# Kernel optimization log

Measured on AMD Instinct MI355X. Metric: run time of the kernel, lower is better.

## Reference

```python
import jax, jax.numpy as jnp
import numpy as np

H = 51  # hidden size fixed by the module

def _gru_cell(x, h, w_ih, w_hh, b_ih, b_hh):
    # PyTorch GRUCell math. w_ih: [3H, in], w_hh: [3H, H]
    gi = x @ w_ih.T + b_ih          # [B, 3H]
    gh = h @ w_hh.T + b_hh          # [B, 3H]
    i_r, i_z, i_n = jnp.split(gi, 3, axis=-1)
    h_r, h_z, h_n = jnp.split(gh, 3, axis=-1)
    r = jax.nn.sigmoid(i_r + h_r)
    z = jax.nn.sigmoid(i_z + h_z)
    n = jnp.tanh(i_n + r * h_n)
    return (1.0 - z) * n + z * h


def setup_inputs() -> dict:
    key = jax.random.key(0)
    ks = jax.random.split(key, 11)
    B, T = 2048, 1000
    s = 1.0 / np.sqrt(H)  # torch default init scale
    u = lambda k, shape: jax.random.uniform(k, shape, jnp.float32, -s, s)
    return {
        "x": jax.random.normal(ks[0], (B, T), jnp.float32),
        "w_ih1": u(ks[1], (3 * H, 1)),
        "w_hh1": u(ks[2], (3 * H, H)),
        "b_ih1": u(ks[3], (3 * H,)),
        "b_hh1": u(ks[4], (3 * H,)),
        "w_ih2": u(ks[5], (3 * H, H)),
        "w_hh2": u(ks[6], (3 * H, H)),
        "b_ih2": u(ks[7], (3 * H,)),
        "b_hh2": u(ks[8], (3 * H,)),
        "w_lin": u(ks[9], (1, H)),
        "b_lin": u(ks[10], (1,)),
        "future_steps": 1000,
    }


def reference(x, w_ih1, w_hh1, b_ih1, b_hh1, w_ih2, w_hh2, b_ih2, b_hh2,
              w_lin, b_lin, future_steps):
    B = x.shape[0]
    h1 = jnp.zeros((B, H), x.dtype)
    h2 = jnp.zeros((B, H), x.dtype)

    def step(carry, xt):  # xt: [B, 1]
        h1, h2 = carry
        h1 = _gru_cell(xt, h1, w_ih1, w_hh1, b_ih1, b_hh1)
        h2 = _gru_cell(h1, h2, w_ih2, w_hh2, b_ih2, b_hh2)
        out = h2 @ w_lin.T + b_lin  # [B, 1]
        return (h1, h2), out

    xs = jnp.swapaxes(x, 0, 1)[:, :, None]  # [T, B, 1]
    (h1, h2), outs1 = jax.lax.scan(step, (h1, h2), xs)

    def fstep(carry, _):
        h1, h2, out = carry
        h1 = _gru_cell(out, h1, w_ih1, w_hh1, b_ih1, b_hh1)
        h2 = _gru_cell(h1, h2, w_ih2, w_hh2, b_ih2, b_hh2)
        out = h2 @ w_lin.T + b_lin
        return (h1, h2, out), out

    last = outs1[-1]
    (_, _, _), outs2 = jax.lax.scan(fstep, (h1, h2, last), None,
                                    length=future_steps)

    outs = jnp.concatenate([outs1, outs2], axis=0)  # [T+F, B, 1]
    return jnp.swapaxes(outs[:, :, 0], 0, 1)        # [B, T+F]
```

## Files before the change

### kernel.cpp

```cpp
#include <hip/hip_runtime.h>
#include <hip/hip_bf16.h>

#define HH 51
#define TPB 512
#define BPB 8
#define US 36

typedef _Float16 half8 __attribute__((ext_vector_type(8)));
typedef float f4 __attribute__((ext_vector_type(4)));

#define LBAR() asm volatile("s_waitcnt lgkmcnt(0)\ns_barrier" ::: "memory")

__device__ __forceinline__ float bf2f(unsigned short u) {
    return __uint_as_float(((unsigned)u) << 16);
}
__device__ __forceinline__ float loadf(const void* p, size_t i, bool bf) {
    return bf ? bf2f(((const unsigned short*)p)[i]) : ((const float*)p)[i];
}
__device__ __forceinline__ void storef(void* p, size_t i, float v, bool bf) {
    if (bf) ((__hip_bfloat16*)p)[i] = __float2bfloat16(v);
    else    ((float*)p)[i] = v;
}
__device__ __forceinline__ float sigm(float v) {
    return __builtin_amdgcn_rcpf(1.0f + __expf(-v));
}
__device__ __forceinline__ float tanh_fast(float v) {
    return fmaf(2.0f, __builtin_amdgcn_rcpf(1.0f + __expf(-2.0f * v)), -1.0f);
}
__device__ __forceinline__ f4 MF(half8 a, half8 b, f4 c) {
    return __builtin_amdgcn_mfma_f32_16x16x32_f16(a, b, c, 0, 0, 0);
}
__device__ __forceinline__ float wave_sum(float x) {
    float s = x, t;
    t = __builtin_bit_cast(float, __builtin_amdgcn_update_dpp(0, __builtin_bit_cast(int, s), 0x111, 0xf, 0xf, true)); s += t;
    t = __builtin_bit_cast(float, __builtin_amdgcn_update_dpp(0, __builtin_bit_cast(int, s), 0x112, 0xf, 0xf, true)); s += t;
    t = __builtin_bit_cast(float, __builtin_amdgcn_update_dpp(0, __builtin_bit_cast(int, s), 0x114, 0xf, 0xf, true)); s += t;
    t = __builtin_bit_cast(float, __builtin_amdgcn_update_dpp(0, __builtin_bit_cast(int, s), 0x118, 0xf, 0xf, true)); s += t;
    t = __builtin_bit_cast(float, __builtin_amdgcn_update_dpp(0, __builtin_bit_cast(int, s), 0x142, 0xa, 0xf, true)); s += t;
    t = __builtin_bit_cast(float, __builtin_amdgcn_update_dpp(0, __builtin_bit_cast(int, s), 0x143, 0xc, 0xf, true)); s += t;
    return __builtin_bit_cast(float, __builtin_amdgcn_readlane(__builtin_bit_cast(int, s), 63));
}
__device__ __forceinline__ float rdlane(float v, int idx) {
    return __builtin_bit_cast(float, __builtin_amdgcn_readlane(__builtin_bit_cast(int, v), idx));
}

__global__ __launch_bounds__(TPB, 1) void gru_kernel(
    const void* __restrict__ xg,
    const void* __restrict__ wih1, const void* __restrict__ whh1,
    const void* __restrict__ bih1, const void* __restrict__ bhh1,
    const void* __restrict__ wih2, const void* __restrict__ whh2,
    const void* __restrict__ bih2, const void* __restrict__ bhh2,
    const void* __restrict__ wlin, const void* __restrict__ blin_p,
    void* __restrict__ dout, int T, int TF)
{
    __shared__ __align__(16) _Float16 stg[208 * 64];
    __shared__ __align__(16) float gbuf1[52 * US];
    __shared__ __align__(16) float gbuf2[52 * US];
    __shared__ __align__(16) _Float16 h1T[2][16 * 72];
    __shared__ __align__(16) _Float16 h2T[2][16 * 72];
    __shared__ float obufL[BPB * 64];
    __shared__ float hfin[2][BPB * 52];

    const int tid = threadIdx.x, w = tid >> 6, lane = tid & 63;
    const int n16 = lane & 15, q = lane >> 4;
    const bool li = lane < HH;
    const int il = li ? lane : HH - 1;
    const int bg0 = blockIdx.x * BPB;
    const int myb = bg0 + w;

    bool isbf;
    {
        const unsigned short* u = (const unsigned short*)whh1;
        int ok = 1;
#pragma unroll
        for (int k = 0; k < 16; ++k) {
            unsigned e = (u[2 * k] >> 7) & 0xFF;
            ok &= (e >= 100 && e <= 125) ? 1 : 0;
        }
        isbf = (ok != 0);
    }

    float wr1 = 0, wz1 = 0, wn1 = 0, wl = 0;
    if (li) {
        wr1 = loadf(wih1, il, isbf);          wz1 = loadf(wih1, HH + il, isbf);
        wn1 = loadf(wih1, 2 * HH + il, isbf); wl = loadf(wlin, il, isbf);
    }
    const float blv = loadf(blin_p, 0, isbf);

    const int nm1 = (w < 5) ? 2 : 1;
    int m2a, m2b, nm2;
    if (w < 2)      { m2a = w + 3; m2b = w + 11; nm2 = 2; }
    else if (w < 5) { m2a = w + 3; m2b = 0;      nm2 = 1; }
    else            { m2a = w - 5; m2b = w + 3;  nm2 = 2; }
    const int m1t[2] = { w, w + 8 };
    const int m2t[2] = { m2a, m2b };
    const int laneoff = q * US + 4 * n16;
    const bool stlane = (n16 < 8);
    const bool outw = (w == 1);

    half8 WfM1[2][2], WfM2[2][4];

#pragma unroll 1
    for (int ps = 0; ps < 3; ++ps) {
        for (int e = tid; e < 208 * 64; e += TPB) {
            int r = e >> 6, k = e & 63;
            int u = r >> 2, g = r & 3;
            float v = 0.0f;
            if (ps == 0) {
                if (u < HH) {
                    if (g < 2) {
                        int gr = g * HH + u;
                        if (k < HH) v = loadf(whh1, (size_t)gr * HH + k, isbf);
                        else if (k == 52) v = loadf(bhh1, gr, isbf) + loadf(bih1, gr, isbf);
                        else if (k == 53) v = loadf(wih1, gr, isbf);
                    } else if (g == 2) {
                        int gr = 2 * HH + u;
                        if (k < HH) v = loadf(whh1, (size_t)gr * HH + k, isbf);
                        else if (k == 52) v = loadf(bhh1, gr, isbf);
                    } else {
                        int gr = 2 * HH + u;
                        if (k == 52) v = loadf(bih1, gr, isbf);
                        else if (k == 53) v = loadf(wih1, gr, isbf);
                    }
                }
            } else if (ps == 1) {
                if (u < HH) {
                    if (g < 2) {
                        int gr = g * HH + u;
                        if (k < HH) v = loadf(whh2, (size_t)gr * HH + k, isbf);
                        else if (k == 52) v = loadf(bhh2, gr, isbf) + loadf(bih2, gr, isbf);
                    } else if (g == 2) {
                        int gr = 2 * HH + u;
                        if (k < HH) v = loadf(whh2, (size_t)gr * HH + k, isbf);
                        else if (k == 52) v = loadf(bhh2, gr, isbf);
                    } else {
                        if (k == 52) v = loadf(bih2, 2 * HH + u, isbf);
                    }
                } else if (r == 204) {
                    if (k < HH) v = loadf(wlin, k, isbf);
                    else if (k == 52) v = blv;
                }
            } else {
                if (u < HH) {
                    if (g < 2) {
                        if (k < HH) v = loadf(wih2, (size_t)(g * HH + u) * HH + k, isbf);
                    } else if (g == 3) {
                        if (k < HH) v = loadf(wih2, (size_t)(2 * HH + u) * HH + k, isbf);
                    }
                }
            }
            stg[e] = (_Float16)v;
        }
        __syncthreads();
        if (ps == 0) {
#pragma unroll
            for (int i = 0; i < 2; ++i) if (i < nm1) {
                int tl = m1t[i];
                WfM1[i][0] = *(const half8*)(stg + (size_t)(16 * tl + n16) * 64 + q * 8);
                WfM1[i][1] = *(const half8*)(stg + (size_t)(16 * tl + n16) * 64 + 32 + q * 8);
            }
        } else if (ps == 1) {
#pragma unroll
            for (int i = 0; i < 2; ++i) if (i < nm2) {
                int tl = m2t[i];
                WfM2[i][0] = *(const half8*)(stg + (size_t)(16 * tl + n16) * 64 + q * 8);
                WfM2[i][1] = *(const half8*)(stg + (size_t)(16 * tl + n16) * 64 + 32 + q * 8);
            }
        } else {
#pragma unroll
            for (int i = 0; i < 2; ++i) if (i < nm2) {
                int tl = m2t[i];
                WfM2[i][2] = *(const half8*)(stg + (size_t)(16 * tl + n16) * 64 + q * 8);
                WfM2[i][3] = *(const half8*)(stg + (size_t)(16 * tl + n16) * 64 + 32 + q * 8);
            }
        }
        __syncthreads();
    }

    for (int e = tid; e < 16 * 72; e += TPB) {
        h1T[0][e] = (_Float16)0; h1T[1][e] = (_Float16)0;
        h2T[0][e] = (_Float16)0; h2T[1][e] = (_Float16)0;
    }
    float xreg = 0.0f, xnext = 0.0f;
    if (lane < T) xreg = loadf(xg, (size_t)myb * T + lane, isbf);
    __syncthreads();
    if (tid < 16) {
        h1T[0][tid * 72 + 52] = (_Float16)1.0f; h1T[1][tid * 72 + 52] = (_Float16)1.0f;
        h2T[0][tid * 72 + 52] = (_Float16)1.0f; h2T[1][tid * 72 + 52] = (_Float16)1.0f;
    }
    if (lane == 0) h1T[1][w * 72 + 53] = (_Float16)rdlane(xreg, 0);
    __syncthreads();

    float h1s[2] = {0.f, 0.f}, h2s[2] = {0.f, 0.f};

    for (int t = 0; t < T; ++t) {
        const _Float16* h1r = h1T[(t + 1) & 1];
        const _Float16* h2r = h2T[(t + 1) & 1];
        _Float16* h1w = h1T[t & 1];
        _Float16* h2w = h2T[t & 1];
        half8 H10 = *(const half8*)(h1r + n16 * 72 + q * 8);
        half8 H11 = *(const half8*)(h1r + n16 * 72 + 32 + q * 8);
        half8 H20 = *(const half8*)(h2r + n16 * 72 + q * 8);
        half8 H21 = *(const half8*)(h2r + n16 * 72 + 32 + q * 8);
        {
            int ni = (t + 1) & 63;
            float xsrc = (ni == 0) ? xnext : xreg;
            float xnv = (t == T - 1) ? 0.0f : rdlane(xsrc, ni);
            if (lane == 0) h1w[w * 72 + 53] = (_Float16)xnv;
        }
#pragma unroll
        for (int i = 0; i < 2; ++i) if (i < nm1) {
            f4 a = {0.f, 0.f, 0.f, 0.f};
            a = MF(WfM1[i][0], H10, a); a = MF(WfM1[i][1], H11, a);
            float r = sigm(a[0]), z = sigm(a[1]);
            float n = tanh_fast(fmaf(r, a[2], a[3]));
            float h = fmaf(z, h1s[i] - n, n); h1s[i] = h;
            int u = 4 * m1t[i] + q;
            if (n16 < 8 && u < HH) h1w[n16 * 72 + u] = (_Float16)h;
        }
#pragma unroll
        for (int i = 0; i < 2; ++i) if (i < nm2) {
            f4 a = {0.f, 0.f, 0.f, 0.f}, b = {0.f, 0.f, 0.f, 0.f};
            a = MF(WfM2[i][0], H20, a); a = MF(WfM2[i][1], H21, a);
            b = MF(WfM2[i][2], H10, b); b = MF(WfM2[i][3], H11, b);
            a = a + b;
            if (t > 0) {
                if (outw && i == 1 && q == 3 && n16 < 8 && t >= 2)
                    obufL[n16 * 64 + ((t - 2) & 63)] = a[0];
                float r2 = sigm(a[0]), z2 = sigm(a[1]);
                float n2 = tanh_fast(fmaf(r2, a[2], a[3]));
                float h = fmaf(z2, h2s[i] - n2, n2); h2s[i] = h;
                int u = 4 * m2t[i] + q;
                if (n16 < 8 && u < HH) h2w[n16 * 72 + u] = (_Float16)h;
            }
        }
        if (w >= 6 && (t & 31) == 2 && t >= 34) {
            int fb = t - 34;
#pragma unroll
            for (int k2 = 0; k2 < 2; ++k2) {
                int et = ((w - 6) << 7) + (k2 << 6) + lane;
                int b2 = et >> 5, tt = et & 31;
                storef(dout, (size_t)(bg0 + b2) * TF + fb + tt, obufL[b2 * 64 + ((fb + tt) & 63)], isbf);
            }
        }
        if ((t & 63) == 0) {
            int base = t + 64;
            if (base < T) {
                int src = base + lane;
                xnext = (src < T) ? loadf(xg, (size_t)myb * T + src, isbf) : 0.0f;
            }
        } else if ((t & 63) == 63) {
            xreg = xnext;
        }
        LBAR();
    }

    const int fbi = (T + 1) & 1;
    {
        const _Float16* h1r = h1T[fbi];
        const _Float16* h2r = h2T[fbi];
        half8 H10 = *(const half8*)(h1r + n16 * 72 + q * 8);
        half8 H11 = *(const half8*)(h1r + n16 * 72 + 32 + q * 8);
        half8 H20 = *(const half8*)(h2r + n16 * 72 + q * 8);
        half8 H21 = *(const half8*)(h2r + n16 * 72 + 32 + q * 8);
#pragma unroll
        for (int i = 0; i < 2; ++i) if (i < nm1) {
            f4 a = {0.f, 0.f, 0.f, 0.f};
            a = MF(WfM1[i][0], H10, a); a = MF(WfM1[i][1], H11, a);
            if (stlane) *(f4*)(gbuf1 + m1t[i] * 4 * US + laneoff) = a;
            int u = 4 * m1t[i] + q;
            if (n16 < 8 && u < HH) hfin[0][n16 * 52 + u] = h1s[i];
        }
#pragma unroll
        for (int i = 0; i < 2; ++i) if (i < nm2) {
            f4 a = {0.f, 0.f, 0.f, 0.f}, b = {0.f, 0.f, 0.f, 0.f};
            a = MF(WfM2[i][0], H20, a); a = MF(WfM2[i][1], H21, a);
            b = MF(WfM2[i][2], H10, b); b = MF(WfM2[i][3], H11, b);
            a = a + b;
            if (stlane) *(f4*)(gbuf2 + m2t[i] * 4 * US + laneoff) = a;
            int u = 4 * m2t[i] + q;
            if (n16 < 8 && u < HH) hfin[1][n16 * 52 + u] = h2s[i];
        }
    }
    __syncthreads();

    float h1p = hfin[0][w * 52 + il];
    float h2p = hfin[1][w * 52 + il];
    const float* gl1 = gbuf1 + il * US + 4 * w;
    const float* gl2 = gbuf2 + il * US + 4 * w;
    const int or2 = 51 * US;
    _Float16* fh1 = h1T[fbi];
    _Float16* fh2 = h2T[fbi];

    for (int t = T; t < TF; ++t) {
        f4 G1 = *(const f4*)gl1;
        f4 G2 = *(const f4*)gl2;
        if (t == T && lane == 0)
            obufL[w * 64 + ((t - 2) & 63)] = gbuf2[or2 + 4 * w];
        {
            float r2 = sigm(G2[0]), z2 = sigm(G2[1]);
            float n2 = tanh_fast(fmaf(r2, G2[2], G2[3]));
            float h = fmaf(z2, h2p - n2, n2); h2p = h;
            float p = 0.0f;
            if (li) {
                fh2[w * 72 + il] = (_Float16)h;
                p = h * wl;
            }
            float outv = wave_sum(p) + blv;
            if (lane == 0) obufL[w * 64 + ((t - 1) & 63)] = outv;
            float r = sigm(fmaf(outv, wr1, G1[0]));
            float z = sigm(fmaf(outv, wz1, G1[1]));
            float n = tanh_fast(fmaf(r, G1[2], fmaf(outv, wn1, G1[3])));
            float h1 = fmaf(z, h1p - n, n); h1p = h1;
            if (li) fh1[w * 72 + il] = (_Float16)h1;
        }
        LBAR();
        {
            half8 H10 = *(const half8*)(fh1 + n16 * 72 + q * 8);
            half8 H11 = *(const half8*)(fh1 + n16 * 72 + 32 + q * 8);
            half8 H20 = *(const half8*)(fh2 + n16 * 72 + q * 8);
            half8 H21 = *(const half8*)(fh2 + n16 * 72 + 32 + q * 8);
#pragma unroll
            for (int i = 0; i < 2; ++i) if (i < nm1) {
                f4 a = {0.f, 0.f, 0.f, 0.f};
                a = MF(WfM1[i][0], H10, a); a = MF(WfM1[i][1], H11, a);
                if (stlane) *(f4*)(gbuf1 + m1t[i] * 4 * US + laneoff) = a;
            }
#pragma unroll
            for (int i = 0; i < 2; ++i) if (i < nm2) {
                f4 a = {0.f, 0.f, 0.f, 0.f}, b = {0.f, 0.f, 0.f, 0.f};
                a = MF(WfM2[i][0], H20, a); a = MF(WfM2[i][1], H21, a);
                b = MF(WfM2[i][2], H10, b); b = MF(WfM2[i][3], H11, b);
                a = a + b;
                if (stlane) *(f4*)(gbuf2 + m2t[i] * 4 * US + laneoff) = a;
            }
        }
        if (w >= 6 && (t & 31) == 0) {
            int fb = t - 32;
#pragma unroll
            for (int k2 = 0; k2 < 2; ++k2) {
                int et = ((w - 6) << 7) + (k2 << 6) + lane;
                int b2 = et >> 5, tt = et & 31;
                storef(dout, (size_t)(bg0 + b2) * TF + fb + tt, obufL[b2 * 64 + ((fb + tt) & 63)], isbf);
            }
        }
        LBAR();
    }

    {
        f4 G2 = *(const f4*)gl2;
        float p = 0.0f;
        float r2 = sigm(G2[0]), z2 = sigm(G2[1]);
        float n2 = tanh_fast(fmaf(r2, G2[2], G2[3]));
        float h = fmaf(z2, h2p - n2, n2);
        if (li) p = h * wl;
        float osum = wave_sum(p) + blv;
        if (lane == 0) obufL[w * 64 + ((TF - 1) & 63)] = osum;
    }
    __syncthreads();
    {
        int base = (TF - 1) & ~31, rem = TF - base;
        if (tid < BPB * 32) {
            int b2 = tid >> 5, tt = tid & 31;
            if (tt < rem)
                storef(dout, (size_t)(bg0 + b2) * TF + base + tt, obufL[b2 * 64 + ((base + tt) & 63)], isbf);
        }
    }
}

extern "C" void kernel_launch(void* const* d_in, const int* in_sizes, int n_in,
                              void* d_out, int out_size, void* d_ws, size_t ws_size,
                              hipStream_t stream) {
    const int B = 2048;
    const int T = in_sizes[0] / B;
    const int TF = out_size / B;
    gru_kernel<<<dim3(B / BPB), dim3(TPB), 0, stream>>>(
        d_in[0], d_in[1], d_in[2], d_in[3], d_in[4], d_in[5],
        d_in[6], d_in[7], d_in[8], d_in[9], d_in[10],
        d_out, T, TF);
}
```

Baseline: 1.609 ms.

## Fuse layer-2 gate activation into MFMA epilogue with partial linear-output reduction

In the autoregressive phase, the layer-2 GRU update now happens right after its MFMA, in the MFMA lane layout, instead of writing gates to a shared buffer and re-reading them per unit. Each wave computes a partial dot product with the output weights, reduces it with shuffles, and writes per-wave partials to a small shared array. The next step sums these partials to get the output, which replaces the 6-step DPP wave reduction on the critical path. Row tiles are rebalanced across waves (layer-1 tiles 1–3 per wave, layer-2 tiles reassigned), and the output writer and flush waves change to match. The aim is to cut shared-memory round trips and serial work per step, at the cost of an uneven per-wave load.

```diff
diff --git a/kernel.cpp b/kernel.cpp
--- a/kernel.cpp
+++ b/kernel.cpp
@@ -29,16 +29,6 @@
 }
 __device__ __forceinline__ f4 MF(half8 a, half8 b, f4 c) {
     return __builtin_amdgcn_mfma_f32_16x16x32_f16(a, b, c, 0, 0, 0);
-}
-__device__ __forceinline__ float wave_sum(float x) {
-    float s = x, t;
-    t = __builtin_bit_cast(float, __builtin_amdgcn_update_dpp(0, __builtin_bit_cast(int, s), 0x111, 0xf, 0xf, true)); s += t;
-    t = __builtin_bit_cast(float, __builtin_amdgcn_update_dpp(0, __builtin_bit_cast(int, s), 0x112, 0xf, 0xf, true)); s += t;
-    t = __builtin_bit_cast(float, __builtin_amdgcn_update_dpp(0, __builtin_bit_cast(int, s), 0x114, 0xf, 0xf, true)); s += t;
-    t = __builtin_bit_cast(float, __builtin_amdgcn_update_dpp(0, __builtin_bit_cast(int, s), 0x118, 0xf, 0xf, true)); s += t;
-    t = __builtin_bit_cast(float, __builtin_amdgcn_update_dpp(0, __builtin_bit_cast(int, s), 0x142, 0xa, 0xf, true)); s += t;
-    t = __builtin_bit_cast(float, __builtin_amdgcn_update_dpp(0, __builtin_bit_cast(int, s), 0x143, 0xc, 0xf, true)); s += t;
-    return __builtin_bit_cast(float, __builtin_amdgcn_readlane(__builtin_bit_cast(int, s), 63));
 }
 __device__ __forceinline__ float rdlane(float v, int idx) {
     return __builtin_bit_cast(float, __builtin_amdgcn_readlane(__builtin_bit_cast(int, v), idx));
@@ -55,11 +45,11 @@
 {
     __shared__ __align__(16) _Float16 stg[208 * 64];
     __shared__ __align__(16) float gbuf1[52 * US];
-    __shared__ __align__(16) float gbuf2[52 * US];
     __shared__ __align__(16) _Float16 h1T[2][16 * 72];
     __shared__ __align__(16) _Float16 h2T[2][16 * 72];
-    __shared__ float obufL[BPB * 64];
-    __shared__ float hfin[2][BPB * 52];
+    __shared__ __align__(16) float obufL[BPB * 64];
+    __shared__ __align__(16) float opart[BPB * 8];
+    __shared__ __align__(16) float hfin[BPB * 52];
 
     const int tid = threadIdx.x, w = tid >> 6, lane = tid & 63;
     const int n16 = lane & 15, q = lane >> 4;
@@ -80,25 +70,30 @@
         isbf = (ok != 0);
     }
 
-    float wr1 = 0, wz1 = 0, wn1 = 0, wl = 0;
+    float wr1 = 0, wz1 = 0, wn1 = 0;
     if (li) {
-        wr1 = loadf(wih1, il, isbf);          wz1 = loadf(wih1, HH + il, isbf);
-        wn1 = loadf(wih1, 2 * HH + il, isbf); wl = loadf(wlin, il, isbf);
+        wr1 = loadf(wih1, il, isbf);  wz1 = loadf(wih1, HH + il, isbf);
+        wn1 = loadf(wih1, 2 * HH + il, isbf);
     }
     const float blv = loadf(blin_p, 0, isbf);
 
-    const int nm1 = (w < 5) ? 2 : 1;
-    int m2a, m2b, nm2;
-    if (w < 2)      { m2a = w + 3; m2b = w + 11; nm2 = 2; }
-    else if (w < 5) { m2a = w + 3; m2b = 0;      nm2 = 1; }
-    else            { m2a = w - 5; m2b = w + 3;  nm2 = 2; }
-    const int m1t[2] = { w, w + 8 };
-    const int m2t[2] = { m2a, m2b };
+    const int nm1 = (w < 5) ? 1 : (w < 7) ? 3 : 2;
+    const int bm1 = (w < 5) ? w : 5 + (w - 5) * 3;
+    int m1t[3] = { bm1, bm1 + 1, bm1 + 2 };
+    const int nm2 = (w < 5) ? 2 : 1;
+    int m2t[2] = { (w < 5) ? 2 * w : w + 5, (w < 5) ? 2 * w + 1 : 0 };
     const int laneoff = q * US + 4 * n16;
     const bool stlane = (n16 < 8);
-    const bool outw = (w == 1);
-
-    half8 WfM1[2][2], WfM2[2][4];
+    const bool outw = (w == 7);
+
+    float wlc[2] = { 0.f, 0.f };
+#pragma unroll
+    for (int i = 0; i < 2; ++i) if (i < nm2) {
+        int u = 4 * m2t[i] + q;
+        if (u < HH) wlc[i] = loadf(wlin, u, isbf);
+    }
+
+    half8 WfM1[3][2], WfM2[2][4];
 
 #pragma unroll 1
     for (int ps = 0; ps < 3; ++ps) {
@@ -154,7 +149,7 @@
         __syncthreads();
         if (ps == 0) {
 #pragma unroll
-            for (int i = 0; i < 2; ++i) if (i < nm1) {
+            for (int i = 0; i < 3; ++i) if (i < nm1) {
                 int tl = m1t[i];
                 WfM1[i][0] = *(const half8*)(stg + (size_t)(16 * tl + n16) * 64 + q * 8);
                 WfM1[i][1] = *(const half8*)(stg + (size_t)(16 * tl + n16) * 64 + 32 + q * 8);
@@ -191,7 +186,7 @@
     if (lane == 0) h1T[1][w * 72 + 53] = (_Float16)rdlane(xreg, 0);
     __syncthreads();
 
-    float h1s[2] = {0.f, 0.f}, h2s[2] = {0.f, 0.f};
+    float h1s[3] = {0.f, 0.f, 0.f}, h2s[2] = {0.f, 0.f};
 
     for (int t = 0; t < T; ++t) {
         const _Float16* h1r = h1T[(t + 1) & 1];
@@ -209,7 +204,7 @@
             if (lane == 0) h1w[w * 72 + 53] = (_Float16)xnv;
         }
 #pragma unroll
-        for (int i = 0; i < 2; ++i) if (i < nm1) {
+        for (int i = 0; i < 3; ++i) if (i < nm1) {
             f4 a = {0.f, 0.f, 0.f, 0.f};
             a = MF(WfM1[i][0], H10, a); a = MF(WfM1[i][1], H11, a);
             float r = sigm(a[0]), z = sigm(a[1]);
@@ -225,7 +220,7 @@
             b = MF(WfM2[i][2], H10, b); b = MF(WfM2[i][3], H11, b);
             a = a + b;
             if (t > 0) {
-                if (outw && i == 1 && q == 3 && n16 < 8 && t >= 2)
+                if (outw && i == 0 && q == 3 && n16 < 8 && t >= 2)
                     obufL[n16 * 64 + ((t - 2) & 63)] = a[0];
                 float r2 = sigm(a[0]), z2 = sigm(a[1]);
                 float n2 = tanh_fast(fmaf(r2, a[2], a[3]));
@@ -234,11 +229,11 @@
                 if (n16 < 8 && u < HH) h2w[n16 * 72 + u] = (_Float16)h;
             }
         }
-        if (w >= 6 && (t & 31) == 2 && t >= 34) {
+        if ((w == 5 || w == 6) && (t & 31) == 2 && t >= 34) {
             int fb = t - 34;
 #pragma unroll
             for (int k2 = 0; k2 < 2; ++k2) {
-                int et = ((w - 6) << 7) + (k2 << 6) + lane;
+                int et = ((w - 5) << 7) + (k2 << 6) + lane;
                 int b2 = et >> 5, tt = et & 31;
                 storef(dout, (size_t)(bg0 + b2) * TF + fb + tt, obufL[b2 * 64 + ((fb + tt) & 63)], isbf);
             }
@@ -263,51 +258,48 @@
         half8 H11 = *(const half8*)(h1r + n16 * 72 + 32 + q * 8);
         half8 H20 = *(const half8*)(h2r + n16 * 72 + q * 8);
         half8 H21 = *(const half8*)(h2r + n16 * 72 + 32 + q * 8);
-#pragma unroll
-        for (int i = 0; i < 2; ++i) if (i < nm1) {
+        _Float16* h2wn = h2T[T & 1];
+#pragma unroll
+        for (int i = 0; i < 3; ++i) if (i < nm1) {
             f4 a = {0.f, 0.f, 0.f, 0.f};
             a = MF(WfM1[i][0], H10, a); a = MF(WfM1[i][1], H11, a);
             if (stlane) *(f4*)(gbuf1 + m1t[i] * 4 * US + laneoff) = a;
             int u = 4 * m1t[i] + q;
-            if (n16 < 8 && u < HH) hfin[0][n16 * 52 + u] = h1s[i];
-        }
+            if (n16 < 8 && u < HH) hfin[n16 * 52 + u] = h1s[i];
+        }
+        float po = 0.0f;
 #pragma unroll
         for (int i = 0; i < 2; ++i) if (i < nm2) {
             f4 a = {0.f, 0.f, 0.f, 0.f}, b = {0.f, 0.f, 0.f, 0.f};
             a = MF(WfM2[i][0], H20, a); a = MF(WfM2[i][1], H21, a);
             b = MF(WfM2[i][2], H10, b); b = MF(WfM2[i][3], H11, b);
             a = a + b;
-            if (stlane) *(f4*)(gbuf2 + m2t[i] * 4 * US + laneoff) = a;
+            if (outw && i == 0 && q == 3 && n16 < 8)
+                obufL[n16 * 64 + ((T - 2) & 63)] = a[0];
+            float r2 = sigm(a[0]), z2 = sigm(a[1]);
+            float n2 = tanh_fast(fmaf(r2, a[2], a[3]));
+            float h = fmaf(z2, h2s[i] - n2, n2); h2s[i] = h;
             int u = 4 * m2t[i] + q;
-            if (n16 < 8 && u < HH) hfin[1][n16 * 52 + u] = h2s[i];
-        }
+            if (n16 < 8 && u < HH) h2wn[n16 * 72 + u] = (_Float16)h;
+            po += h * wlc[i];
+        }
+        po += __shfl_xor(po, 16);
+        po += __shfl_xor(po, 32);
+        if (lane < 8) opart[lane * 8 + w] = po;
     }
     __syncthreads();
 
-    float h1p = hfin[0][w * 52 + il];
-    float h2p = hfin[1][w * 52 + il];
+    float h1p = hfin[w * 52 + il];
     const float* gl1 = gbuf1 + il * US + 4 * w;
-    const float* gl2 = gbuf2 + il * US + 4 * w;
-    const int or2 = 51 * US;
     _Float16* fh1 = h1T[fbi];
-    _Float16* fh2 = h2T[fbi];
 
     for (int t = T; t < TF; ++t) {
         f4 G1 = *(const f4*)gl1;
-        f4 G2 = *(const f4*)gl2;
-        if (t == T && lane == 0)
-            obufL[w * 64 + ((t - 2) & 63)] = gbuf2[or2 + 4 * w];
+        f4 pa = *(const f4*)(opart + w * 8);
+        f4 pb = *(const f4*)(opart + w * 8 + 4);
+        float outv = ((pa[0] + pa[1]) + (pa[2] + pa[3])) + ((pb[0] + pb[1]) + (pb[2] + pb[3])) + blv;
+        if (lane == 0) obufL[w * 64 + ((t - 1) & 63)] = outv;
         {
-            float r2 = sigm(G2[0]), z2 = sigm(G2[1]);
-            float n2 = tanh_fast(fmaf(r2, G2[2], G2[3]));
-            float h = fmaf(z2, h2p - n2, n2); h2p = h;
-            float p = 0.0f;
-            if (li) {
-                fh2[w * 72 + il] = (_Float16)h;
-                p = h * wl;
-            }
-            float outv = wave_sum(p) + blv;
-            if (lane == 0) obufL[w * 64 + ((t - 1) & 63)] = outv;
             float r = sigm(fmaf(outv, wr1, G1[0]));
             float z = sigm(fmaf(outv, wz1, G1[1]));
             float n = tanh_fast(fmaf(r, G1[2], fmaf(outv, wn1, G1[3])));
@@ -318,28 +310,39 @@
         {
             half8 H10 = *(const half8*)(fh1 + n16 * 72 + q * 8);
             half8 H11 = *(const half8*)(fh1 + n16 * 72 + 32 + q * 8);
-            half8 H20 = *(const half8*)(fh2 + n16 * 72 + q * 8);
-            half8 H21 = *(const half8*)(fh2 + n16 * 72 + 32 + q * 8);
-#pragma unroll
-            for (int i = 0; i < 2; ++i) if (i < nm1) {
+            const _Float16* h2r = h2T[t & 1];
+            half8 H20 = *(const half8*)(h2r + n16 * 72 + q * 8);
+            half8 H21 = *(const half8*)(h2r + n16 * 72 + 32 + q * 8);
+            _Float16* h2wn = h2T[(t + 1) & 1];
+#pragma unroll
+            for (int i = 0; i < 3; ++i) if (i < nm1) {
                 f4 a = {0.f, 0.f, 0.f, 0.f};
                 a = MF(WfM1[i][0], H10, a); a = MF(WfM1[i][1], H11, a);
                 if (stlane) *(f4*)(gbuf1 + m1t[i] * 4 * US + laneoff) = a;
             }
+            float po = 0.0f;
 #pragma unroll
             for (int i = 0; i < 2; ++i) if (i < nm2) {
                 f4 a = {0.f, 0.f, 0.f, 0.f}, b = {0.f, 0.f, 0.f, 0.f};
                 a = MF(WfM2[i][0], H20, a); a = MF(WfM2[i][1], H21, a);
                 b = MF(WfM2[i][2], H10, b); b = MF(WfM2[i][3], H11, b);
                 a = a + b;
-                if (stlane) *(f4*)(gbuf2 + m2t[i] * 4 * US + laneoff) = a;
-            }
-        }
-        if (w >= 6 && (t & 31) == 0) {
+                float r2 = sigm(a[0]), z2 = sigm(a[1]);
+                float n2 = tanh_fast(fmaf(r2, a[2], a[3]));
+                float h = fmaf(z2, h2s[i] - n2, n2); h2s[i] = h;
+                int u = 4 * m2t[i] + q;
+                if (n16 < 8 && u < HH) h2wn[n16 * 72 + u] = (_Float16)h;
+                po += h * wlc[i];
+            }
+            po += __shfl_xor(po, 16);
+            po += __shfl_xor(po, 32);
+            if (lane < 8) opart[lane * 8 + w] = po;
+        }
+        if ((w == 5 || w == 6) && (t & 31) == 0) {
             int fb = t - 32;
 #pragma unroll
             for (int k2 = 0; k2 < 2; ++k2) {
-                int et = ((w - 6) << 7) + (k2 << 6) + lane;
+                int et = ((w - 5) << 7) + (k2 << 6) + lane;
                 int b2 = et >> 5, tt = et & 31;
                 storef(dout, (size_t)(bg0 + b2) * TF + fb + tt, obufL[b2 * 64 + ((fb + tt) & 63)], isbf);
             }
@@ -348,14 +351,10 @@
     }
 
     {
-        f4 G2 = *(const f4*)gl2;
-        float p = 0.0f;
-        float r2 = sigm(G2[0]), z2 = sigm(G2[1]);
-        float n2 = tanh_fast(fmaf(r2, G2[2], G2[3]));
-        float h = fmaf(z2, h2p - n2, n2);
-        if (li) p = h * wl;
-        float osum = wave_sum(p) + blv;
-        if (lane == 0) obufL[w * 64 + ((TF - 1) & 63)] = osum;
+        f4 pa = *(const f4*)(opart + w * 8);
+        f4 pb = *(const f4*)(opart + w * 8 + 4);
+        float outv = ((pa[0] + pa[1]) + (pa[2] + pa[3])) + ((pb[0] + pb[1]) + (pb[2] + pb[3])) + blv;
+        if (lane == 0) obufL[w * 64 + ((TF - 1) & 63)] = outv;
     }
     __syncthreads();
     {
```

After: 1.726 ms. +7.3%, slower.
